# Kernel optimization log

Hardware: AMD Instinct MI355X
Metric: run time of the kernel (lower is better)

## Reference

```python
import jax, jax.numpy as jnp
import numpy as np

N, E, B, T, F, H, O = 50000, 800000, 16, 4, 128, 128, 128
LEAKY = 0.2  # PyG GATConv negative_slope default


def setup_inputs() -> dict:
    key = jax.random.key(0)
    ks = jax.random.split(key, 12)
    s = 0.05
    return {
        "x": jax.random.normal(ks[0], (T, N, F), jnp.float32),
        "edge_index": jax.random.randint(ks[1], (2, E), 0, N, dtype=jnp.int32),
        "batch_idx": jnp.sort(jax.random.randint(ks[2], (N,), 0, B, dtype=jnp.int32)),
        "W1": jax.random.normal(ks[3], (F, H), jnp.float32) * s,
        "att_src1": jax.random.normal(ks[4], (H,), jnp.float32) * s,
        "att_dst1": jax.random.normal(ks[5], (H,), jnp.float32) * s,
        "b1": jnp.zeros((H,), jnp.float32),
        "W2": jax.random.normal(ks[6], (H, O), jnp.float32) * s,
        "att_src2": jax.random.normal(ks[7], (O,), jnp.float32) * s,
        "att_dst2": jax.random.normal(ks[8], (O,), jnp.float32) * s,
        "b2": jnp.zeros((O,), jnp.float32),
    }


def gat_layer(h, src, dst, W, a_src, a_dst, b):
    # PyG GATConv, heads=1, concat=False, self-loops already appended.
    h = h @ W                                  # [N, out]
    alpha_s = h @ a_src                        # [N]
    alpha_d = h @ a_dst                        # [N]
    e = alpha_s[src] + alpha_d[dst]            # [E']
    e = jnp.where(e > 0, e, LEAKY * e)         # leaky_relu
    # softmax over incoming edges of each destination node (every node has a self-loop)
    m = jax.ops.segment_max(e, dst, num_segments=N)
    ex = jnp.exp(e - m[dst])
    z = jax.ops.segment_sum(ex, dst, num_segments=N)
    alpha = ex / z[dst]                        # [E']
    out = jax.ops.segment_sum(alpha[:, None] * h[src], dst, num_segments=N)
    return out + b


def reference(x, edge_index, batch_idx, W1, att_src1, att_dst1, b1, W2, att_src2, att_dst2, b2):
    loops = jnp.arange(N, dtype=edge_index.dtype)
    src = jnp.concatenate([edge_index[0], loops])  # add_self_loops (PyG default)
    dst = jnp.concatenate([edge_index[1], loops])
    ones = jnp.ones((N, 1), jnp.float32)
    cnt = jax.ops.segment_sum(ones, batch_idx, num_segments=B)  # [B,1]

    def per_snapshot(xt):
        h = gat_layer(xt, src, dst, W1, att_src1, att_dst1, b1)
        h = jax.nn.relu(h)                     # inter-layer ReLU (dropout=0, eval)
        h = gat_layer(h, src, dst, W2, att_src2, att_dst2, b2)
        return jax.ops.segment_sum(h, batch_idx, num_segments=B) / cnt  # mean pool [B,O]

    reps = jax.vmap(per_snapshot)(x)           # [T, B, O]
    return jnp.transpose(reps, (1, 0, 2))      # [B, T, O]
```

## Files before the change

kernel.cpp:

```cpp
#include <hip/hip_runtime.h>
#include <hip/hip_bf16.h>

#define LEAKY 0.2f

typedef __attribute__((ext_vector_type(8))) short bf16x8;
typedef __attribute__((ext_vector_type(4))) float f32x4;
typedef __attribute__((ext_vector_type(2))) float f32x2;


__global__ __launch_bounds__(256) void k_init(int* cnt, int* bstart, int n, int nb) {
    int i = blockIdx.x * 256 + threadIdx.x;
    if (i < n) cnt[i] = 1;
    if (i < nb) bstart[i] = n;
}

__global__ __launch_bounds__(256) void k_count(const int* __restrict__ dst, int* cnt, int e,
                                               const int* __restrict__ bidx, int* bstart, int n) {
    int i = blockIdx.x * 256 + threadIdx.x;
    if (i < e) atomicAdd(&cnt[dst[i]], 1);
    if (i < n) {
        int b = bidx[i];
        if (i == 0 || bidx[i - 1] != b) atomicMin(&bstart[b], i);
    }
}

__device__ inline int block_incl_scan(int v, int* lds) {
    int lane = threadIdx.x & 63, wid = threadIdx.x >> 6;
    int s = v;
#pragma unroll
    for (int o = 1; o < 64; o <<= 1) { int t = __shfl_up(s, o); if (lane >= o) s += t; }
    if (lane == 63) lds[wid] = s;
    __syncthreads();
    int add = 0;
#pragma unroll
    for (int ww = 0; ww < 3; ++ww) if (ww < wid) add += lds[ww];
    return s + add;
}

__global__ __launch_bounds__(256) void k_scanA(const int* __restrict__ cnt, int* bsum, int n) {
    __shared__ int lds[4];
    int i = blockIdx.x * 256 + threadIdx.x;
    int v = (i < n) ? ((cnt[i] + 15) & ~15) : 0;
    int s = block_incl_scan(v, lds);
    if (threadIdx.x == 255) bsum[blockIdx.x] = s;
}

__global__ __launch_bounds__(256) void k_scanB(int* bsum, int* boff, int nb,
                                               int* bstart, int n, int nbatch) {
    __shared__ int lds[4];
    int i = threadIdx.x;
    int v = (i < nb) ? bsum[i] : 0;
    int s = block_incl_scan(v, lds);
    if (i < nb) boff[i] = s - v;
    if (i == 0) {
        bstart[nbatch] = n;
        for (int b = nbatch - 1; b >= 0; --b)
            if (bstart[b] == n) bstart[b] = bstart[b + 1];
    }
}

__global__ __launch_bounds__(256) void k_scanC(const int* __restrict__ cnt, const int* __restrict__ boff,
                                               int* row_ptr, int* csr, int* cursor, int n) {
    __shared__ int lds[4];
    int i = blockIdx.x * 256 + threadIdx.x;
    int v = (i < n) ? ((cnt[i] + 15) & ~15) : 0;
    int s = block_incl_scan(v, lds) + boff[blockIdx.x];
    if (i < n) {
        int excl = s - v;
        row_ptr[i + 1] = s;
        csr[excl] = i;
        cursor[i] = excl + 1;
    }
    if (i == 0) row_ptr[0] = 0;
}

__global__ __launch_bounds__(256) void k_scatter(const int* __restrict__ src, const int* __restrict__ dst,
                                                 int* cursor, int* csr, int e) {
    int i = blockIdx.x * 256 + threadIdx.x;
    if (i < e) { int p = atomicAdd(&cursor[dst[i]], 1); csr[p] = src[i]; }
}

__global__ __launch_bounds__(256) void k_pad(const int* __restrict__ row_ptr, const int* __restrict__ cursor,
                                             int* csr, int n) {
    int i = blockIdx.x * 256 + threadIdx.x;
    if (i >= n) return;
    int p = cursor[i], e = row_ptr[i + 1];
    int v = i | 0x80000000;
    for (; p < e; ++p) csr[p] = v;
}

__device__ inline unsigned short bf16r(float x) {
    unsigned int u = __float_as_uint(x);
    u += 0x7fffu + ((u >> 16) & 1u);
    return (unsigned short)(u >> 16);
}

__device__ inline unsigned int bfpair(float lo, float hi) {
    unsigned int ul = __float_as_uint(lo); ul += 0x7fffu + ((ul >> 16) & 1u);
    unsigned int uh = __float_as_uint(hi); uh += 0x7fffu + ((uh >> 16) & 1u);
    return (ul >> 16) | (uh & 0xffff0000u);
}

template <bool ABF16>
__global__ __launch_bounds__(256) void k_gemm_mfma(
    const void* __restrict__ Asrc, const float* __restrict__ W,
    const float* __restrict__ asrc, const float* __restrict__ adst,
    unsigned char* __restrict__ hq, float* __restrict__ vas, float* __restrict__ vad,
    int nrows)
{
    __shared__ unsigned short Wt[128 * 136];
    int tid = threadIdx.x;
    int lane = tid & 63, wv = tid >> 6;
    int row0 = blockIdx.x * 128;
    int c0 = lane & 15, g = lane >> 4;

    {
        int k = tid >> 1;
        int n0 = (tid & 1) * 64;
        const float4* wr = (const float4*)&W[k * 128 + n0];
#pragma unroll
        for (int i = 0; i < 16; ++i) {
            float4 v = wr[i];
            int n = n0 + i * 4;
            Wt[(n + 0) * 136 + k] = bf16r(v.x);
            Wt[(n + 1) * 136 + k] = bf16r(v.y);
            Wt[(n + 2) * 136 + k] = bf16r(v.z);
            Wt[(n + 3) * 136 + k] = bf16r(v.w);
        }
    }
    __syncthreads();

    f32x4 acc[2][8];
#pragma unroll
    for (int mi = 0; mi < 2; ++mi)
#pragma unroll
        for (int ni = 0; ni < 8; ++ni)
#pragma unroll
            for (int q = 0; q < 4; ++q) acc[mi][ni][q] = 0.f;

    int rA[2];
#pragma unroll
    for (int mi = 0; mi < 2; ++mi)
        rA[mi] = min(row0 + wv * 32 + mi * 16 + c0, nrows - 1);

#pragma unroll
    for (int ks = 0; ks < 4; ++ks) {
        int k0 = ks * 32;
        bf16x8 af[2];
#pragma unroll
        for (int mi = 0; mi < 2; ++mi) {
            if (ABF16) {
                af[mi] = *(const bf16x8*)((const unsigned short*)Asrc + (size_t)rA[mi] * 128 + k0 + g * 8);
            } else {
                const float4* ap = (const float4*)((const float*)Asrc + (size_t)rA[mi] * 128 + k0 + g * 8);
                float4 f0 = ap[0], f1 = ap[1];
                uint4 p = make_uint4(bfpair(f0.x, f0.y), bfpair(f0.z, f0.w),
                                     bfpair(f1.x, f1.y), bfpair(f1.z, f1.w));
                af[mi] = *(bf16x8*)&p;
            }
        }
        bf16x8 bfr[8];
#pragma unroll
        for (int ni = 0; ni < 8; ++ni)
            bfr[ni] = *(const bf16x8*)&Wt[(ni * 16 + c0) * 136 + k0 + g * 8];
#pragma unroll
        for (int mi = 0; mi < 2; ++mi)
#pragma unroll
            for (int ni = 0; ni < 8; ++ni)
                acc[mi][ni] = __builtin_amdgcn_mfma_f32_16x16x32_bf16(bfr[ni], af[mi], acc[mi][ni], 0, 0, 0);
    }

    float4 as4[8], ad4[8];
#pragma unroll
    for (int ni = 0; ni < 8; ++ni) {
        as4[ni] = *(const float4*)&asrc[ni * 16 + g * 4];
        ad4[ni] = *(const float4*)&adst[ni * 16 + g * 4];
    }
#pragma unroll
    for (int mi = 0; mi < 2; ++mi) {
        int node = row0 + wv * 32 + mi * 16 + c0;
        bool ok = node < nrows;
        float s = 0.f, d = 0.f;
        unsigned packs[8];
#pragma unroll
        for (int ni = 0; ni < 8; ++ni) {
            f32x4 vv = acc[mi][ni];
            s = fmaf(vv[0], as4[ni].x, fmaf(vv[1], as4[ni].y, fmaf(vv[2], as4[ni].z, fmaf(vv[3], as4[ni].w, s))));
            d = fmaf(vv[0], ad4[ni].x, fmaf(vv[1], ad4[ni].y, fmaf(vv[2], ad4[ni].z, fmaf(vv[3], ad4[ni].w, d))));
            unsigned p0 = (unsigned)__builtin_amdgcn_cvt_pk_fp8_f32(vv[0], vv[1], 0, false);
            packs[ni] = (unsigned)__builtin_amdgcn_cvt_pk_fp8_f32(vv[2], vv[3], (int)p0, true);
        }
        s += __shfl_xor(s, 16); s += __shfl_xor(s, 32);
        d += __shfl_xor(d, 16); d += __shfl_xor(d, 32);
        if (ok) {
            if (g == 0) { vas[node] = s; vad[node] = d; }
#pragma unroll
            for (int ni = 0; ni < 8; ++ni)
                *(unsigned*)&hq[(size_t)node * 128 + ni * 16 + g * 4] = packs[ni];
        }
    }
}

template <bool RELU>
__global__ __launch_bounds__(256) void k_agg(const unsigned char* __restrict__ hq,
                                             const float* __restrict__ vas,
                                             const float* __restrict__ vad,
                                             const int* __restrict__ row_ptr,
                                             const int* __restrict__ csr,
                                             const float* __restrict__ bias,
                                             unsigned int* __restrict__ outb,
                                             int n, int chunksPerT) {
    int i = blockIdx.x;
    int slot = i & 7;
    int t = slot >> 1;
    int chunk = ((i >> 3) << 1) | (slot & 1);
    if (chunk >= chunksPerT) return;
    int tid = threadIdx.x;
    int grp = tid >> 4, l = tid & 15;
    int w = chunk * 16 + grp;
    if (w >= n) return;
    unsigned int tbase = (unsigned int)t * (unsigned int)n;
    unsigned int g = tbase + (unsigned int)w;
    int beg = row_ptr[w], end = row_ptr[w + 1];
    float advl = vad[g];

    f32x2 acc2[4];
#pragma unroll
    for (int q = 0; q < 4; ++q) { acc2[q].x = 0.f; acc2[q].y = 0.f; }
    float zp = 0.f;

    for (int c = beg; c < end; c += 16) {
        int raw = csr[c + l];
        unsigned int s_l = tbase + (unsigned int)(raw & 0x7fffffff);
        float e = vas[s_l] + advl;
        e = e > 0.f ? e : LEAKY * e;
        float w_l = (raw >= 0) ? __expf(e) : 0.f;
        zp += w_l;

        unsigned int ofs[16]; float wt[16];
#pragma unroll
        for (int q = 0; q < 16; ++q) {
            ofs[q] = __shfl(s_l, q, 16) * 128u + (unsigned int)(l * 8);
            wt[q] = __shfl(w_l, q, 16);
        }
        uint2 v[16];
#pragma unroll
        for (int q = 0; q < 16; ++q)
            v[q] = *(const uint2*)&hq[ofs[q]];
#pragma unroll
        for (int q = 0; q < 16; ++q) {
            f32x2 w2; w2.x = wt[q]; w2.y = wt[q];
            acc2[0] = __builtin_elementwise_fma(w2, __builtin_amdgcn_cvt_pk_f32_fp8(v[q].x, false), acc2[0]);
            acc2[1] = __builtin_elementwise_fma(w2, __builtin_amdgcn_cvt_pk_f32_fp8(v[q].x, true),  acc2[1]);
            acc2[2] = __builtin_elementwise_fma(w2, __builtin_amdgcn_cvt_pk_f32_fp8(v[q].y, false), acc2[2]);
            acc2[3] = __builtin_elementwise_fma(w2, __builtin_amdgcn_cvt_pk_f32_fp8(v[q].y, true),  acc2[3]);
        }
    }

    float z = zp;
#pragma unroll
    for (int o = 1; o < 16; o <<= 1) z += __shfl_xor(z, o, 16);
    float inv = 1.0f / z;

    float4 b0 = *(const float4*)&bias[l * 8];
    float4 b1 = *(const float4*)&bias[l * 8 + 4];
    float4 o0 = make_float4(fmaf(acc2[0].x, inv, b0.x), fmaf(acc2[0].y, inv, b0.y),
                            fmaf(acc2[1].x, inv, b0.z), fmaf(acc2[1].y, inv, b0.w));
    float4 o1 = make_float4(fmaf(acc2[2].x, inv, b1.x), fmaf(acc2[2].y, inv, b1.y),
                            fmaf(acc2[3].x, inv, b1.z), fmaf(acc2[3].y, inv, b1.w));
    if (RELU) {
        o0.x = fmaxf(o0.x, 0.f); o0.y = fmaxf(o0.y, 0.f); o0.z = fmaxf(o0.z, 0.f); o0.w = fmaxf(o0.w, 0.f);
        o1.x = fmaxf(o1.x, 0.f); o1.y = fmaxf(o1.y, 0.f); o1.z = fmaxf(o1.z, 0.f); o1.w = fmaxf(o1.w, 0.f);
    }
    uint4 p = make_uint4(bfpair(o0.x, o0.y), bfpair(o0.z, o0.w),
                         bfpair(o1.x, o1.y), bfpair(o1.z, o1.w));
    *(uint4*)&outb[(size_t)g * 64 + l * 4] = p;
}

__global__ __launch_bounds__(128) void k_pool(const unsigned int* __restrict__ h,
                                              const int* __restrict__ bstart,
                                              float* __restrict__ out, int n, int T) {
    int b = blockIdx.x;
    int chunk = blockIdx.y;
    int t = blockIdx.z;
    int f = threadIdx.x;
    int s = bstart[b], e = bstart[b + 1];
    int cnt = e - s;
    if (cnt <= 0) return;
    int len = (cnt + 31) / 32;
    int cs = s + chunk * len;
    int ce = min(cs + len, e);
    if (cs >= ce) return;
    const unsigned int* ht = h + (size_t)t * n * 64;
    float acc = 0.f;
    for (int nidx = cs; nidx < ce; ++nidx) {
        unsigned int v = ht[(size_t)nidx * 64 + (f >> 1)];
        acc += __uint_as_float((f & 1) ? (v & 0xffff0000u) : (v << 16));
    }
    atomicAdd(&out[(size_t)(b * T + t) * 128 + f], acc / (float)cnt);
}


extern "C" void kernel_launch(void* const* d_in, const int* in_sizes, int n_in,
                              void* d_out, int out_size, void* d_ws, size_t ws_size,
                              hipStream_t stream) {
    const float* x    = (const float*)d_in[0];
    const int*   ei   = (const int*)d_in[1];
    const int*   bidx = (const int*)d_in[2];
    const float* W1   = (const float*)d_in[3];
    const float* as1  = (const float*)d_in[4];
    const float* ad1  = (const float*)d_in[5];
    const float* b1   = (const float*)d_in[6];
    const float* W2   = (const float*)d_in[7];
    const float* as2  = (const float*)d_in[8];
    const float* ad2  = (const float*)d_in[9];
    const float* b2   = (const float*)d_in[10];
    float* out = (float*)d_out;

    const int E = in_sizes[1] / 2;
    const int N = in_sizes[2];
    const int T = in_sizes[0] / (N * 128);
    const int B = out_size / (T * 128);
    const int* src = ei;
    const int* dst = ei + E;
    const int NT = N * T;

    char* wsp = (char*)d_ws;
    auto alloc = [&](size_t bytes) { void* p = wsp; wsp += (bytes + 255) / 256 * 256; return p; };
    unsigned char* hq    = (unsigned char*)alloc((size_t)NT * 128);
    unsigned int* hb2    = (unsigned int*)alloc((size_t)NT * 64 * 4);
    float* vas           = (float*)alloc((size_t)NT * 4);
    float* vad           = (float*)alloc((size_t)NT * 4);
    int* row_ptr         = (int*)alloc((size_t)(N + 1) * 4);
    int* cnt             = (int*)alloc((size_t)N * 4);
    int* csr             = (int*)alloc(((size_t)E + 16ull * N + 64) * 4);
    int* bstart          = (int*)alloc((size_t)(B + 2) * 4);
    int  nScanB          = (N + 255) / 256;
    int* bsum            = (int*)alloc((size_t)nScanB * 4);
    int* boff            = (int*)alloc((size_t)nScanB * 4);

    hipMemsetAsync(d_out, 0, (size_t)out_size * sizeof(float), stream);

    int gN = (N + 255) / 256, gE = (E + 255) / 256;
    k_init<<<gN, 256, 0, stream>>>(cnt, bstart, N, B + 1);
    k_count<<<gE, 256, 0, stream>>>(dst, cnt, E, bidx, bstart, N);
    k_scanA<<<nScanB, 256, 0, stream>>>(cnt, bsum, N);
    k_scanB<<<1, 256, 0, stream>>>(bsum, boff, nScanB, bstart, N, B);
    k_scanC<<<nScanB, 256, 0, stream>>>(cnt, boff, row_ptr, csr, cnt, N);
    k_scatter<<<gE, 256, 0, stream>>>(src, dst, cnt, csr, E);
    k_pad<<<gN, 256, 0, stream>>>(row_ptr, cnt, csr, N);

    int gGemm = (NT + 127) / 128;
    int chunksPerT = (N + 15) / 16;
    int chunksPad = ((chunksPerT + 1) / 2) * 2;
    int gAggFlat = chunksPad * 4;
    k_gemm_mfma<false><<<gGemm, 256, 0, stream>>>(x,   W1, as1, ad1, hq, vas, vad, NT);
    k_agg<true ><<<gAggFlat, 256, 0, stream>>>(hq, vas, vad, row_ptr, csr, b1, hb2, N, chunksPerT);
    k_gemm_mfma<true ><<<gGemm, 256, 0, stream>>>(hb2, W2, as2, ad2, hq, vas, vad, NT);
    k_agg<false><<<gAggFlat, 256, 0, stream>>>(hq, vas, vad, row_ptr, csr, b2, hb2, N, chunksPerT);
    k_pool<<<dim3(B, 32, T), 128, 0, stream>>>(hb2, bstart, out, N, T);
}
```

Measured before the change: 351.1 us.

## Bucket destination nodes by padded degree to balance aggregation work

Builds a degree histogram during the CSR scan, then a prefix over 32 buckets, and a permutation that groups nodes by padded degree. The aggregation kernels map each 16-lane group to a node taken from that permutation, so groups in the same block have similar edge counts and less divergence. The cost is an extra tiny serial kernel, atomics during padding, and an indirection that loses node locality for output writes and vad reads. Atomic ordering inside a bucket is nondeterministic, but results are unaffected.

Result: slower. 1.118 ms (+218.4%).

```diff
diff --git a/kernel.cpp b/kernel.cpp
--- a/kernel.cpp
+++ b/kernel.cpp
@@ -8,10 +8,11 @@
 typedef __attribute__((ext_vector_type(2))) float f32x2;
 
 
-__global__ __launch_bounds__(256) void k_init(int* cnt, int* bstart, int n, int nb) {
+__global__ __launch_bounds__(256) void k_init(int* cnt, int* bstart, int* hist, int n, int nb) {
     int i = blockIdx.x * 256 + threadIdx.x;
     if (i < n) cnt[i] = 1;
     if (i < nb) bstart[i] = n;
+    if (i < 32) hist[i] = 0;
 }
 
 __global__ __launch_bounds__(256) void k_count(const int* __restrict__ dst, int* cnt, int e,
@@ -60,7 +61,7 @@
 }
 
 __global__ __launch_bounds__(256) void k_scanC(const int* __restrict__ cnt, const int* __restrict__ boff,
-                                               int* row_ptr, int* csr, int* cursor, int n) {
+                                               int* row_ptr, int* csr, int* cursor, int* hist, int n) {
     __shared__ int lds[4];
     int i = blockIdx.x * 256 + threadIdx.x;
     int v = (i < n) ? ((cnt[i] + 15) & ~15) : 0;
@@ -70,6 +71,7 @@
         row_ptr[i + 1] = s;
         csr[excl] = i;
         cursor[i] = excl + 1;
+        atomicAdd(&hist[min(v >> 4, 31)], 1);
     }
     if (i == 0) row_ptr[0] = 0;
 }
@@ -80,11 +82,19 @@
     if (i < e) { int p = atomicAdd(&cursor[dst[i]], 1); csr[p] = src[i]; }
 }
 
+__global__ void k_bscan(const int* __restrict__ hist, int* bcur) {
+    int run = 0;
+    for (int b = 0; b < 32; ++b) { bcur[b] = run; run += hist[b]; }
+}
+
 __global__ __launch_bounds__(256) void k_pad(const int* __restrict__ row_ptr, const int* __restrict__ cursor,
-                                             int* csr, int n) {
+                                             int* csr, int* bcur, int* perm, int n) {
     int i = blockIdx.x * 256 + threadIdx.x;
     if (i >= n) return;
-    int p = cursor[i], e = row_ptr[i + 1];
+    int b0 = row_ptr[i], p = cursor[i], e = row_ptr[i + 1];
+    int bkt = min((e - b0) >> 4, 31);
+    int pos = atomicAdd(&bcur[bkt], 1);
+    perm[pos] = i;
     int v = i | 0x80000000;
     for (; p < e; ++p) csr[p] = v;
 }
@@ -207,6 +217,7 @@
                                              const float* __restrict__ vad,
                                              const int* __restrict__ row_ptr,
                                              const int* __restrict__ csr,
+                                             const int* __restrict__ perm,
                                              const float* __restrict__ bias,
                                              unsigned int* __restrict__ outb,
                                              int n, int chunksPerT) {
@@ -217,8 +228,9 @@
     if (chunk >= chunksPerT) return;
     int tid = threadIdx.x;
     int grp = tid >> 4, l = tid & 15;
-    int w = chunk * 16 + grp;
-    if (w >= n) return;
+    int idx = chunk * 16 + grp;
+    if (idx >= n) return;
+    int w = perm[idx];
     unsigned int tbase = (unsigned int)t * (unsigned int)n;
     unsigned int g = tbase + (unsigned int)w;
     int beg = row_ptr[w], end = row_ptr[w + 1];
@@ -334,6 +346,9 @@
     int* row_ptr         = (int*)alloc((size_t)(N + 1) * 4);
     int* cnt             = (int*)alloc((size_t)N * 4);
     int* csr             = (int*)alloc(((size_t)E + 16ull * N + 64) * 4);
+    int* perm            = (int*)alloc((size_t)N * 4);
+    int* hist            = (int*)alloc(32 * 4);
+    int* bcur            = (int*)alloc(32 * 4);
     int* bstart          = (int*)alloc((size_t)(B + 2) * 4);
     int  nScanB          = (N + 255) / 256;
     int* bsum            = (int*)alloc((size_t)nScanB * 4);
@@ -342,21 +357,22 @@
     hipMemsetAsync(d_out, 0, (size_t)out_size * sizeof(float), stream);
 
     int gN = (N + 255) / 256, gE = (E + 255) / 256;
-    k_init<<<gN, 256, 0, stream>>>(cnt, bstart, N, B + 1);
+    k_init<<<gN, 256, 0, stream>>>(cnt, bstart, hist, N, B + 1);
     k_count<<<gE, 256, 0, stream>>>(dst, cnt, E, bidx, bstart, N);
     k_scanA<<<nScanB, 256, 0, stream>>>(cnt, bsum, N);
     k_scanB<<<1, 256, 0, stream>>>(bsum, boff, nScanB, bstart, N, B);
-    k_scanC<<<nScanB, 256, 0, stream>>>(cnt, boff, row_ptr, csr, cnt, N);
+    k_scanC<<<nScanB, 256, 0, stream>>>(cnt, boff, row_ptr, csr, cnt, hist, N);
     k_scatter<<<gE, 256, 0, stream>>>(src, dst, cnt, csr, E);
-    k_pad<<<gN, 256, 0, stream>>>(row_ptr, cnt, csr, N);
+    k_bscan<<<1, 1, 0, stream>>>(hist, bcur);
+    k_pad<<<gN, 256, 0, stream>>>(row_ptr, cnt, csr, bcur, perm, N);
 
     int gGemm = (NT + 127) / 128;
     int chunksPerT = (N + 15) / 16;
     int chunksPad = ((chunksPerT + 1) / 2) * 2;
     int gAggFlat = chunksPad * 4;
     k_gemm_mfma<false><<<gGemm, 256, 0, stream>>>(x,   W1, as1, ad1, hq, vas, vad, NT);
-    k_agg<true ><<<gAggFlat, 256, 0, stream>>>(hq, vas, vad, row_ptr, csr, b1, hb2, N, chunksPerT);
+    k_agg<true ><<<gAggFlat, 256, 0, stream>>>(hq, vas, vad, row_ptr, csr, perm, b1, hb2, N, chunksPerT);
     k_gemm_mfma<true ><<<gGemm, 256, 0, stream>>>(hb2, W2, as2, ad2, hq, vas, vad, NT);
-    k_agg<false><<<gAggFlat, 256, 0, stream>>>(hq, vas, vad, row_ptr, csr, b2, hb2, N, chunksPerT);
+    k_agg<false><<<gAggFlat, 256, 0, stream>>>(hq, vas, vad, row_ptr, csr, perm, b2, hb2, N, chunksPerT);
     k_pool<<<dim3(B, 32, T), 128, 0, stream>>>(hb2, bstart, out, N, T);
 }
```
